# Performance work log

Measured on AMD Instinct MI355X. Metric: run time of the kernel, lower is better.

Reference implementation:

```python
import jax, jax.numpy as jnp
import numpy as np
import math

D_MODEL = 512

def setup_inputs() -> dict:
    key = jax.random.key(0)
    k1, k2, k3 = jax.random.split(key, 3)
    X = jax.random.normal(k1, (4, 8192, D_MODEL), dtype=jnp.float32)
    # nn.Linear(d, d, bias=False) weights, applied as x @ W.T
    s = 1.0 / math.sqrt(D_MODEL)
    W_v = jax.random.uniform(k2, (D_MODEL, D_MODEL), dtype=jnp.float32, minval=-s, maxval=s)
    W_theta = jax.random.uniform(k3, (D_MODEL, D_MODEL), dtype=jnp.float32, minval=-s, maxval=s)
    return {"X": X, "W_v": W_v, "W_theta": W_theta}

def reference(X, W_v, W_theta):
    # X: [B, n, d]
    n = X.shape[1]
    d = X.shape[2]
    XW_v = X @ W_v.T            # [B, n, d]
    theta_X = X @ W_theta.T     # [B, n, d]
    # first term: (1/n) * ones(n,n) @ XW_v == column mean broadcast over rows
    first_term = jnp.mean(XW_v, axis=1, keepdims=True)  # [B, 1, d], broadcasts
    # second term: (1/(n*sqrt(d))) * (X @ theta_X^T) @ XW_v
    # associativity-reduced: theta_X^T @ XW_v is [B, d, d]
    kv = jnp.einsum('bnd,bne->bde', theta_X, XW_v)       # [B, d, d]
    second_term = (X @ kv) / (n * math.sqrt(d))          # [B, n, d]
    return first_term + second_term
```

## Files before the change

kernel.cpp:

```cpp
#include <hip/hip_runtime.h>
#include <stdint.h>


typedef __bf16 bf16x8 __attribute__((ext_vector_type(8)));
typedef float f32x4 __attribute__((ext_vector_type(4)));
typedef unsigned short u16x4 __attribute__((ext_vector_type(4)));
typedef unsigned short u16x8 __attribute__((ext_vector_type(8)));

#define BK 32

#define VM0 asm volatile("s_waitcnt vmcnt(0)" ::: "memory")
#define BAR asm volatile("s_barrier" ::: "memory")

template <int N>
__device__ __forceinline__ void vmw() {
  if constexpr (N == 0) asm volatile("s_waitcnt vmcnt(0)" ::: "memory");
  else if constexpr (N == 1) asm volatile("s_waitcnt vmcnt(1)" ::: "memory");
  else if constexpr (N == 2) asm volatile("s_waitcnt vmcnt(2)" ::: "memory");
  else if constexpr (N == 4) asm volatile("s_waitcnt vmcnt(4)" ::: "memory");
  else if constexpr (N == 8) asm volatile("s_waitcnt vmcnt(8)" ::: "memory");
}

__device__ __forceinline__ unsigned short f2bf(float f) {
  union { float f; unsigned int u; } c; c.f = f;
  unsigned int u = c.u;
  return (unsigned short)((u + 0x7FFFu + ((u >> 16) & 1u)) >> 16);
}
__device__ __forceinline__ float bf2f(unsigned short h) {
  union { unsigned int u; float f; } c; c.u = ((unsigned int)h) << 16;
  return c.f;
}

__device__ __forceinline__ void gld16(const void* g, void* l) {
  using gptr_t = const __attribute__((address_space(1))) void*;
  using lptr_t = __attribute__((address_space(3))) void*;
  __builtin_amdgcn_global_load_lds((gptr_t)(uintptr_t)g,
                                   (lptr_t)(uint32_t)(uintptr_t)l, 16, 0, 0);
}

template <int TB>
__device__ __forceinline__ void gemm_tile(const unsigned short* __restrict__ A, int lda,
                                          const unsigned short* __restrict__ B, int ldb,
                                          int K, int m0, int n0,
                                          f32x4 (&acc)[TB / 32][TB / 32], bool sameAB) {
  static_assert(TB == 64 || TB == 128, "TB");
  constexpr int FR = TB / 32;
  constexpr int LPT = TB / 32;
  constexpr int LJ = (TB * 4) / 256;
  __shared__ unsigned short sA[2][TB * BK];
  __shared__ unsigned short sB[2][TB * BK];
  const int tid = threadIdx.x;
  const int lane = tid & 63;
  const int w = tid >> 6;
  const int wm = w >> 1, wn = w & 1;
  const int quad = lane >> 4, l16 = lane & 15;

#pragma unroll
  for (int mi = 0; mi < FR; mi++)
#pragma unroll
    for (int ni = 0; ni < FR; ni++) acc[mi][ni] = f32x4{0.f, 0.f, 0.f, 0.f};

  auto stage = [&](int bb, int kk) {
#pragma unroll
    for (int j = 0; j < LJ; j++) {
      const int slot = w * (LJ * 64) + j * 64 + lane;
      const int row = slot >> 2;
      const int col = (slot & 3) * 8;
      const int base = w * (LJ * 64) + j * 64;
      gld16(A + (size_t)(m0 + row) * lda + kk + col, (char*)sA[bb] + (size_t)base * 16);
      if (!sameAB)
        gld16(B + (size_t)(n0 + row) * ldb + kk + col, (char*)sB[bb] + (size_t)base * 16);
    }
  };

  auto compute = [&](int bb) {
    const unsigned short* as = sA[bb];
    const unsigned short* bs = sameAB ? sA[bb] : sB[bb];
    bf16x8 af[FR], bfr[FR];
#pragma unroll
    for (int mi = 0; mi < FR; mi++)
      af[mi] = *(const bf16x8*)&as[(wm * (TB / 2) + mi * 16 + l16) * BK + quad * 8];
#pragma unroll
    for (int ni = 0; ni < FR; ni++)
      bfr[ni] = *(const bf16x8*)&bs[(wn * (TB / 2) + ni * 16 + l16) * BK + quad * 8];
#pragma unroll
    for (int mi = 0; mi < FR; mi++)
#pragma unroll
      for (int ni = 0; ni < FR; ni++)
        acc[mi][ni] = __builtin_amdgcn_mfma_f32_16x16x32_bf16(af[mi], bfr[ni],
                                                              acc[mi][ni], 0, 0, 0);
  };

  stage(0, 0);
  for (int kt = 0; kt < K; kt += 2 * BK) {
    stage(1, kt + BK);
    if (sameAB) { vmw<LJ>(); } else { vmw<2 * LJ>(); }
    BAR;
    compute(0);
    BAR;
    if (kt + 2 * BK < K) {
      stage(0, kt + 2 * BK);
      if (sameAB) { vmw<LJ>(); } else { vmw<2 * LJ>(); }
    } else {
      VM0;
    }
    BAR;
    compute(1);
    BAR;
  }
}

__global__ __launch_bounds__(256) void prep_kernel(const float* __restrict__ X,
                                                   unsigned short* __restrict__ Xb,
                                                   unsigned short* __restrict__ Xt,
                                                   float* __restrict__ mean_x) {
  __shared__ unsigned short sT[2][64 * 64];
  const int t = threadIdx.x;
  const int n0 = blockIdx.x * 128, d0 = blockIdx.y * 64;
  const int b = n0 >> 13, nb = n0 & 8191;
  const int r0 = (t >> 4) * 4, c0 = (t & 15) * 4;
  f32x4 v[2][4];
#pragma unroll
  for (int s = 0; s < 2; s++)
#pragma unroll
    for (int i = 0; i < 4; i++)
      v[s][i] = *(const f32x4*)(X + (size_t)(n0 + s * 64 + r0 + i) * 512 + d0 + c0);
  __builtin_amdgcn_sched_barrier(0);
  u16x4 o[2][4];
#pragma unroll
  for (int s = 0; s < 2; s++)
#pragma unroll
    for (int i = 0; i < 4; i++)
#pragma unroll
      for (int j = 0; j < 4; j++) o[s][i][j] = f2bf(v[s][i][j]);
#pragma unroll
  for (int s = 0; s < 2; s++)
#pragma unroll
    for (int j = 0; j < 4; j++) {
      u16x4 wv;
#pragma unroll
      for (int i = 0; i < 4; i++) wv[i] = o[s][i][j];
      const int c = c0 + j;
      const int rsw = r0 ^ (c & 0x38);
      *(u16x4*)&sT[s][c * 64 + rsw] = wv;
    }
  __syncthreads();
#pragma unroll
  for (int s = 0; s < 2; s++)
#pragma unroll
    for (int i = 0; i < 4; i++)
      *(u16x4*)(Xb + (size_t)(n0 + s * 64 + r0 + i) * 512 + d0 + c0) = o[s][i];
  const int cr = t >> 3, p = t & 7;
  float csum[2] = {0.f, 0.f};
#pragma unroll
  for (int s = 0; s < 2; s++)
#pragma unroll
    for (int h = 0; h < 2; h++) {
      const int c = cr + h * 32;
      const int phys = (p * 8) ^ (c & 0x38);
      u16x8 val = *(const u16x8*)&sT[s][c * 64 + phys];
      *(u16x8*)(Xt + (size_t)(b * 512 + d0 + c) * 8192 + nb + s * 64 + p * 8) = val;
      float ss = 0.f;
#pragma unroll
      for (int j = 0; j < 8; j++) ss += bf2f(val[j]);
      csum[h] += ss;
    }
#pragma unroll
  for (int h = 0; h < 2; h++) {
    float sv = csum[h];
    sv += __shfl_xor(sv, 1);
    sv += __shfl_xor(sv, 2);
    sv += __shfl_xor(sv, 4);
    if (p == 0) atomicAdd(&mean_x[b * 512 + d0 + cr + h * 32], sv);
  }
}

__global__ __launch_bounds__(256) void prep_w_kernel(const float* __restrict__ Wv,
                                                     const float* __restrict__ Wth,
                                                     unsigned short* __restrict__ Wvb,
                                                     unsigned short* __restrict__ Wtb,
                                                     float* __restrict__ mean_x) {
  const int blk = blockIdx.x;
  const int t = threadIdx.x;
  if (blk == 0) {
#pragma unroll
    for (int i = 0; i < 8; i++) mean_x[t + i * 256] = 0.f;
  }
  const float* src = (blk < 128) ? Wv : Wth;
  unsigned short* dst = (blk < 128) ? Wvb : Wtb;
  const int i = (blk & 127) * 256 + t;
  const f32x4* pp = (const f32x4*)(src + (size_t)i * 8);
  f32x4 v0 = pp[0], v1 = pp[1];
  u16x8 o;
  o[0] = f2bf(v0[0]); o[1] = f2bf(v0[1]); o[2] = f2bf(v0[2]); o[3] = f2bf(v0[3]);
  o[4] = f2bf(v1[0]); o[5] = f2bf(v1[1]); o[6] = f2bf(v1[2]); o[7] = f2bf(v1[3]);
  *(u16x8*)(dst + (size_t)i * 8) = o;
}

static __device__ const int TI[10] = {0, 0, 0, 0, 1, 1, 1, 2, 2, 3};
static __device__ const int TJ[10] = {0, 1, 2, 3, 1, 2, 3, 2, 3, 3};

__global__ __launch_bounds__(256) void g_gemm_kernel(const unsigned short* __restrict__ Xt,
                                                     float* __restrict__ G_part) {
  const int t = blockIdx.x;
  const int z = blockIdx.y;
  const int b = z >> 4, s = z & 15;
  const int m0 = TI[t] * 128, n0 = TJ[t] * 128;
  const unsigned short* A = Xt + (size_t)b * 512 * 8192 + (size_t)s * 512;
  f32x4 acc[4][4];
  gemm_tile<128>(A, 8192, A, 8192, 512, m0, n0, acc, m0 == n0);
  float* Cp = G_part + ((size_t)z * 10 + t) * 16384;
  const int tid = threadIdx.x, lane = tid & 63, w = tid >> 6;
  const int wm = w >> 1, wn = w & 1, quad = lane >> 4, l16 = lane & 15;
#pragma unroll
  for (int mi = 0; mi < 4; mi++)
#pragma unroll
    for (int ni = 0; ni < 4; ni++) {
      const int ml = wm * 64 + mi * 16 + quad * 4;
      const int nl = wn * 64 + ni * 16 + l16;
      *(f32x4*)(Cp + (size_t)nl * 128 + ml) = acc[mi][ni];
    }
}

__global__ __launch_bounds__(256) void g_fin_kernel(const float* __restrict__ G_part,
                                                    unsigned short* __restrict__ Gb,
                                                    const float* __restrict__ mean_x,
                                                    const float* __restrict__ Wv,
                                                    float* __restrict__ meanV) {
  const int blk = blockIdx.x;
  if (blk >= 320) {
    const int idx = (blk - 320) * 256 + threadIdx.x;
    const int b = idx >> 9, e = idx & 511;
    const float* mx = mean_x + b * 512;
    const float* wr = Wv + (size_t)e * 512;
    float s = 0.f;
    for (int d = 0; d < 512; d += 4) {
      f32x4 a = *(const f32x4*)(mx + d);
      f32x4 w4 = *(const f32x4*)(wr + d);
      s += a[0] * w4[0] + a[1] * w4[1] + a[2] * w4[2] + a[3] * w4[3];
    }
    meanV[idx] = s * (1.f / 8192.f);
    return;
  }
  const int b = blk / 80, rem = blk % 80;
  const int t = rem >> 3, cc = rem & 7;
  const int i = TI[t], j = TJ[t];
  const int m0 = i * 128, n0 = j * 128;
  const int tid = threadIdx.x;
  const int np = cc * 16 + (tid >> 4);
  const int mp = (tid & 15) * 8;
  f32x4 s0 = f32x4{0.f, 0.f, 0.f, 0.f}, s1 = f32x4{0.f, 0.f, 0.f, 0.f};
#pragma unroll
  for (int s = 0; s < 16; s++) {
    const float* p = G_part + (((size_t)(b * 16 + s)) * 10 + t) * 16384 + (size_t)np * 128 + mp;
    s0 += *(const f32x4*)p;
    s1 += *(const f32x4*)(p + 4);
  }
  const float scale = (float)(1.0 / (8192.0 * 22.627416997969522));
  unsigned short h[8];
#pragma unroll
  for (int r = 0; r < 4; r++) { h[r] = f2bf(s0[r] * scale); h[r + 4] = f2bf(s1[r] * scale); }
  unsigned short* Gbb = Gb + (size_t)b * 262144;
#pragma unroll
  for (int r = 0; r < 8; r++)
    Gbb[(size_t)(m0 + mp + r) * 512 + (n0 + np)] = h[r];
  if (i != j) {
    u16x8 o;
#pragma unroll
    for (int r = 0; r < 8; r++) o[r] = h[r];
    *(u16x8*)(Gbb + (size_t)(n0 + np) * 512 + (m0 + mp)) = o;
  }
}

__global__ __launch_bounds__(256) void gemm_rm_kernel(const unsigned short* __restrict__ A,
                                                      const unsigned short* __restrict__ B,
                                                      unsigned short* __restrict__ C,
                                                      size_t Abs, size_t Bbs) {
  const int b = blockIdx.z;
  const int m0 = blockIdx.x * 64, n0 = blockIdx.y * 64;
  f32x4 acc[2][2];
  gemm_tile<64>(A + (size_t)b * Abs, 512, B + (size_t)b * Bbs, 512, 512, m0, n0, acc, false);
  unsigned short* Cb = C + (size_t)b * 262144;
  const int tid = threadIdx.x, lane = tid & 63, w = tid >> 6;
  const int wm = w >> 1, wn = w & 1, quad = lane >> 4, l16 = lane & 15;
#pragma unroll
  for (int mi = 0; mi < 2; mi++)
#pragma unroll
    for (int ni = 0; ni < 2; ni++) {
      const int m = m0 + wm * 32 + mi * 16 + quad * 4;
      const int n = n0 + wn * 32 + ni * 16 + l16;
#pragma unroll
      for (int r = 0; r < 4; r++)
        Cb[(size_t)(m + r) * 512 + n] = f2bf(acc[mi][ni][r]);
    }
}

__global__ __launch_bounds__(256) void gemm_out_kernel(
    const unsigned short* __restrict__ Xb, const unsigned short* __restrict__ kvt,
    const float* __restrict__ meanV, float* __restrict__ out) {
  const int m0 = blockIdx.x * 128, n0 = blockIdx.y * 128;
  const int b = blockIdx.x >> 6;
  const unsigned short* Bm = kvt + (size_t)b * 262144;
  f32x4 acc[4][4];
  gemm_tile<128>(Xb, 512, Bm, 512, 512, m0, n0, acc, false);
  const int tid = threadIdx.x, lane = tid & 63, w = tid >> 6;
  const int wm = w >> 1, wn = w & 1, quad = lane >> 4, l16 = lane & 15;
#pragma unroll
  for (int ni = 0; ni < 4; ni++) {
    const int e = n0 + wn * 64 + ni * 16 + l16;
    const float mu = meanV[b * 512 + e];
#pragma unroll
    for (int mi = 0; mi < 4; mi++) {
      const int m = m0 + wm * 64 + mi * 16 + quad * 4;
#pragma unroll
      for (int r = 0; r < 4; r++)
        out[(size_t)(m + r) * 512 + e] = acc[mi][ni][r] + mu;
    }
  }
}

extern "C" void kernel_launch(void* const* d_in, const int* in_sizes, int n_in,
                              void* d_out, int out_size, void* d_ws, size_t ws_size,
                              hipStream_t stream) {
  const float* X = (const float*)d_in[0];
  const float* Wv = (const float*)d_in[1];
  const float* Wth = (const float*)d_in[2];
  float* out = (float*)d_out;
  char* ws = (char*)d_ws;

  unsigned short* Xb = (unsigned short*)(ws);
  unsigned short* Xt = (unsigned short*)(ws + 33554432ull);
  float* G_part = (float*)(ws + 67108864ull);
  unsigned short* Gb = (unsigned short*)(ws + 109051904ull);
  unsigned short* Ht = (unsigned short*)(ws + 111149056ull);
  unsigned short* kvt = (unsigned short*)(ws + 113246208ull);
  unsigned short* Wvb = (unsigned short*)(ws + 115343360ull);
  unsigned short* Wtb = (unsigned short*)(ws + 115867648ull);
  float* mean_x = (float*)(ws + 116391936ull);
  float* meanV = (float*)(ws + 116400128ull);

  prep_w_kernel<<<256, 256, 0, stream>>>(Wv, Wth, Wvb, Wtb, mean_x);
  prep_kernel<<<dim3(256, 8), 256, 0, stream>>>(X, Xb, Xt, mean_x);

  g_gemm_kernel<<<dim3(10, 64), 256, 0, stream>>>(Xt, G_part);
  g_fin_kernel<<<328, 256, 0, stream>>>(G_part, Gb, mean_x, Wv, meanV);

  gemm_rm_kernel<<<dim3(8, 8, 4), 256, 0, stream>>>(Wvb, Gb, Ht, 0, 262144);
  gemm_rm_kernel<<<dim3(8, 8, 4), 256, 0, stream>>>(Ht, Wtb, kvt, 262144, 0);

  gemm_out_kernel<<<dim3(256, 4), 256, 0, stream>>>(Xb, kvt, meanV, out);
}
```

Baseline: 237.9 us.

## Triple-buffer GEMM tile loads and XOR-swizzle LDS layout to avoid bank conflicts

```diff
diff --git a/kernel.cpp b/kernel.cpp
--- a/kernel.cpp
+++ b/kernel.cpp
@@ -9,11 +9,11 @@
 
 #define BK 32
 
-#define VM0 asm volatile("s_waitcnt vmcnt(0)" ::: "memory")
 #define BAR asm volatile("s_barrier" ::: "memory")
 
 template <int N>
 __device__ __forceinline__ void vmw() {
+  static_assert(N == 0 || N == 1 || N == 2 || N == 4 || N == 8, "vmw");
   if constexpr (N == 0) asm volatile("s_waitcnt vmcnt(0)" ::: "memory");
   else if constexpr (N == 1) asm volatile("s_waitcnt vmcnt(1)" ::: "memory");
   else if constexpr (N == 2) asm volatile("s_waitcnt vmcnt(2)" ::: "memory");
@@ -38,51 +38,53 @@
                                    (lptr_t)(uint32_t)(uintptr_t)l, 16, 0, 0);
 }
 
-template <int TB>
+template <int TB, bool SAME>
 __device__ __forceinline__ void gemm_tile(const unsigned short* __restrict__ A, int lda,
                                           const unsigned short* __restrict__ B, int ldb,
-                                          int K, int m0, int n0,
-                                          f32x4 (&acc)[TB / 32][TB / 32], bool sameAB) {
+                                          int m0, int n0, f32x4 (&acc)[TB / 32][TB / 32]) {
   static_assert(TB == 64 || TB == 128, "TB");
   constexpr int FR = TB / 32;
-  constexpr int LPT = TB / 32;
   constexpr int LJ = (TB * 4) / 256;
-  __shared__ unsigned short sA[2][TB * BK];
-  __shared__ unsigned short sB[2][TB * BK];
+  constexpr int LPS = SAME ? LJ : 2 * LJ;
+  constexpr int NK = 512 / BK;
+  __shared__ unsigned short sA[3][TB * BK];
+  __shared__ unsigned short sB[3][TB * BK];
   const int tid = threadIdx.x;
   const int lane = tid & 63;
   const int w = tid >> 6;
   const int wm = w >> 1, wn = w & 1;
   const int quad = lane >> 4, l16 = lane & 15;
+  const int sq = (quad ^ ((l16 >> 1) & 3)) * 8;
 
 #pragma unroll
   for (int mi = 0; mi < FR; mi++)
 #pragma unroll
     for (int ni = 0; ni < FR; ni++) acc[mi][ni] = f32x4{0.f, 0.f, 0.f, 0.f};
 
-  auto stage = [&](int bb, int kk) {
+  auto stage = [&](int bb, int kt) {
+    const int kk = kt * BK;
 #pragma unroll
     for (int j = 0; j < LJ; j++) {
       const int slot = w * (LJ * 64) + j * 64 + lane;
       const int row = slot >> 2;
-      const int col = (slot & 3) * 8;
-      const int base = w * (LJ * 64) + j * 64;
-      gld16(A + (size_t)(m0 + row) * lda + kk + col, (char*)sA[bb] + (size_t)base * 16);
-      if (!sameAB)
-        gld16(B + (size_t)(n0 + row) * ldb + kk + col, (char*)sB[bb] + (size_t)base * 16);
+      const int col = ((slot & 3) ^ ((slot >> 3) & 3)) * 8;
+      const int basegr = w * (LJ * 64) + j * 64;
+      gld16(A + (size_t)(m0 + row) * lda + kk + col, (char*)sA[bb] + (size_t)basegr * 16);
+      if constexpr (!SAME)
+        gld16(B + (size_t)(n0 + row) * ldb + kk + col, (char*)sB[bb] + (size_t)basegr * 16);
     }
   };
 
   auto compute = [&](int bb) {
     const unsigned short* as = sA[bb];
-    const unsigned short* bs = sameAB ? sA[bb] : sB[bb];
+    const unsigned short* bs = SAME ? sA[bb] : sB[bb];
     bf16x8 af[FR], bfr[FR];
 #pragma unroll
     for (int mi = 0; mi < FR; mi++)
-      af[mi] = *(const bf16x8*)&as[(wm * (TB / 2) + mi * 16 + l16) * BK + quad * 8];
+      af[mi] = *(const bf16x8*)&as[(wm * (TB / 2) + mi * 16 + l16) * BK + sq];
 #pragma unroll
     for (int ni = 0; ni < FR; ni++)
-      bfr[ni] = *(const bf16x8*)&bs[(wn * (TB / 2) + ni * 16 + l16) * BK + quad * 8];
+      bfr[ni] = *(const bf16x8*)&bs[(wn * (TB / 2) + ni * 16 + l16) * BK + sq];
 #pragma unroll
     for (int mi = 0; mi < FR; mi++)
 #pragma unroll
@@ -92,21 +94,17 @@
   };
 
   stage(0, 0);
-  for (int kt = 0; kt < K; kt += 2 * BK) {
-    stage(1, kt + BK);
-    if (sameAB) { vmw<LJ>(); } else { vmw<2 * LJ>(); }
+  stage(1, 1);
+  stage(2, 2);
+#pragma unroll
+  for (int kt = 0; kt < NK; ++kt) {
+    if (kt < NK - 2) { vmw<2 * LPS>(); }
+    else if (kt == NK - 2) { vmw<LPS>(); }
+    else { vmw<0>(); }
     BAR;
-    compute(0);
+    compute(kt % 3);
     BAR;
-    if (kt + 2 * BK < K) {
-      stage(0, kt + 2 * BK);
-      if (sameAB) { vmw<LJ>(); } else { vmw<2 * LJ>(); }
-    } else {
-      VM0;
-    }
-    BAR;
-    compute(1);
-    BAR;
+    if (kt < NK - 3) stage(kt % 3, kt + 3);
   }
 }
 
@@ -208,7 +206,10 @@
   const int m0 = TI[t] * 128, n0 = TJ[t] * 128;
   const unsigned short* A = Xt + (size_t)b * 512 * 8192 + (size_t)s * 512;
   f32x4 acc[4][4];
-  gemm_tile<128>(A, 8192, A, 8192, 512, m0, n0, acc, m0 == n0);
+  if (m0 == n0)
+    gemm_tile<128, true>(A, 8192, A, 8192, m0, n0, acc);
+  else
+    gemm_tile<128, false>(A, 8192, A, 8192, m0, n0, acc);
   float* Cp = G_part + ((size_t)z * 10 + t) * 16384;
   const int tid = threadIdx.x, lane = tid & 63, w = tid >> 6;
   const int wm = w >> 1, wn = w & 1, quad = lane >> 4, l16 = lane & 15;
@@ -279,7 +280,7 @@
   const int b = blockIdx.z;
   const int m0 = blockIdx.x * 64, n0 = blockIdx.y * 64;
   f32x4 acc[2][2];
-  gemm_tile<64>(A + (size_t)b * Abs, 512, B + (size_t)b * Bbs, 512, 512, m0, n0, acc, false);
+  gemm_tile<64, false>(A + (size_t)b * Abs, 512, B + (size_t)b * Bbs, 512, m0, n0, acc);
   unsigned short* Cb = C + (size_t)b * 262144;
   const int tid = threadIdx.x, lane = tid & 63, w = tid >> 6;
   const int wm = w >> 1, wn = w & 1, quad = lane >> 4, l16 = lane & 15;
@@ -302,7 +303,7 @@
   const int b = blockIdx.x >> 6;
   const unsigned short* Bm = kvt + (size_t)b * 262144;
   f32x4 acc[4][4];
-  gemm_tile<128>(Xb, 512, Bm, 512, 512, m0, n0, acc, false);
+  gemm_tile<128, false>(Xb, 512, Bm, 512, m0, n0, acc);
   const int tid = threadIdx.x, lane = tid & 63, w = tid >> 6;
   const int wm = w >> 1, wn = w & 1, quad = lane >> 4, l16 = lane & 15;
 #pragma unroll
```

Result: no change. 235.1 us (-1.2%).
